# Kernel tuning notes

Measured on AMD Instinct MI355X. Metric: run time of the kernel, lower is better.

Reference implementation:

```python
import jax, jax.numpy as jnp
import numpy as np

B, L, C = 32, 64, 4


def setup_inputs() -> dict:
    key = jax.random.key(0)
    k_idx, k0, k1, k2, k3 = jax.random.split(key, 5)
    # One-hot encoded sequences, flattened to (B, L*C) as the layer expects.
    idx = jax.random.randint(k_idx, (B, L), 0, C)
    x_lc = jax.nn.one_hot(idx, C, dtype=jnp.float32).reshape(B, L * C)
    return {
        "x_lc": x_lc,
        "theta_0": jnp.zeros((1,), dtype=jnp.float32),  # Constant(0.0) init
        "theta_1": 0.05 * jax.random.normal(k1, (L, C), dtype=jnp.float32),
        "theta_2": 0.05 * jax.random.normal(k2, (L, C, L, C), dtype=jnp.float32),
        "theta_3": 0.05 * jax.random.normal(k3, (L, C, L, C, L, C), dtype=jnp.float32),
    }


def reference(x_lc, theta_0, theta_1, theta_2, theta_3):
    Lp, Cp = theta_1.shape
    xr = x_lc.reshape(-1, Lp, Cp)  # (B, L, C)
    pos = jnp.arange(Lp)
    # strict upper-triangular position masks: l0 < l1 (< l2)
    m2 = (pos[None, :] > pos[:, None]).astype(theta_2.dtype)      # (L, L)
    m3 = m2[:, :, None] * m2[None, :, :]                           # (L, L, L)
    # order 1: sum_{l,c} theta_1[l,c] x[b,l,c]
    phi = theta_0[0] + jnp.einsum('ua,bua->b', theta_1, xr)
    # order 2: sum over l0<l1 of theta_2 * x x
    phi = phi + jnp.einsum('uavc,uv,bua,bvc->b', theta_2, m2, xr, xr)
    # order 3: sum over l0<l1<l2 of theta_3 * x x x
    phi = phi + jnp.einsum('uavcwe,uvw,bua,bvc,bwe->b', theta_3, m3, xr, xr, xr)
    return phi.reshape(-1, 1)
```

## Files before the change

kernel.cpp:

```cpp
#include <hip/hip_runtime.h>

#define BB 32
#define LL 64
#define LC 256
#define NPAIR 2016
#define PPB 4
#define NBLK (NPAIR / PPB)


__global__ __launch_bounds__(256) void init_kernel(
    const float* __restrict__ x, const float* __restrict__ t0,
    const float* __restrict__ t1, float* __restrict__ out)
{
    const int tid = threadIdx.x;
    const int b = tid >> 3, k = tid & 7;
    const float4* __restrict__ x4 = (const float4*)x + b * 64;
    float s = 0.0f;
#pragma unroll
    for (int m = 0; m < 8; ++m) {
        const int l = 8 * m + k;
        float4 f = x4[l];
        int c = 0; float best = f.x;
        if (f.y > best) { best = f.y; c = 1; }
        if (f.z > best) { best = f.z; c = 2; }
        if (f.w > best) { best = f.w; c = 3; }
        s += t1[4 * l + c];
    }
    s += __shfl_down(s, 4, 8);
    s += __shfl_down(s, 2, 8);
    s += __shfl_down(s, 1, 8);
    if (k == 0) out[b] = s + t0[0];
}

__global__ __launch_bounds__(256) void pair_kernel(
    const float* __restrict__ x, const float* __restrict__ t2,
    const float* __restrict__ t3, float* __restrict__ out)
{
    const int tid = threadIdx.x;
    const int b = tid >> 3, k = tid & 7;
    const float4* __restrict__ x4 = (const float4*)x + b * 64;

    int c[8];
#pragma unroll
    for (int m = 0; m < 8; ++m) {
        float4 f = x4[8 * m + k];
        int ci = 0; float best = f.x;
        if (f.y > best) { best = f.y; ci = 1; }
        if (f.z > best) { best = f.z; ci = 2; }
        if (f.w > best) { best = f.w; ci = 3; }
        c[m] = ci;
    }

    const int tp0 = blockIdx.x * PPB;
    int v = (int)((1.0f + sqrtf(8.0f * (float)tp0 + 1.0f)) * 0.5f);
    while (v * (v - 1) / 2 > tp0) --v;
    while ((v + 1) * v / 2 <= tp0) ++v;
    int u = tp0 - v * (v - 1) / 2;

    float acc = 0.0f;
#pragma unroll
    for (int i = 0; i < PPB; ++i) {
        float4 fu = x4[u], fv = x4[v];
        int cu = 0; { float bst = fu.x;
            if (fu.y > bst) { bst = fu.y; cu = 1; }
            if (fu.z > bst) { bst = fu.z; cu = 2; }
            if (fu.w > bst) { bst = fu.w; cu = 3; } }
        int cv = 0; { float bst = fv.x;
            if (fv.y > bst) { bst = fv.y; cv = 1; }
            if (fv.z > bst) { bst = fv.z; cv = 2; }
            if (fv.w > bst) { bst = fv.w; cv = 3; } }
        const int pu = 4 * u + cu, pv = 4 * v + cv;

        const float4* __restrict__ row4 =
            (const float4*)(t3 + ((size_t)pu << 16) + ((size_t)pv << 8));
        if (k == 0) acc += t2[pu * LC + pv];

#pragma unroll
        for (int m = 0; m < 8; ++m) {
            const int w = 8 * m + k;
            float4 f = row4[w];
            const int ci = c[m];
            float lo = (ci & 1) ? f.y : f.x;
            float hi = (ci & 1) ? f.w : f.z;
            float val = (ci & 2) ? hi : lo;
            acc += (w > v) ? val : 0.0f;
        }

        ++u; if (u == v) { u = 0; ++v; }
    }

    acc += __shfl_down(acc, 4, 8);
    acc += __shfl_down(acc, 2, 8);
    acc += __shfl_down(acc, 1, 8);
    if (k == 0) atomicAdd(&out[b], acc);
}

extern "C" void kernel_launch(void* const* d_in, const int* in_sizes, int n_in,
                              void* d_out, int out_size, void* d_ws, size_t ws_size,
                              hipStream_t stream) {
    const float* x  = (const float*)d_in[0];
    const float* t0 = (const float*)d_in[1];
    const float* t1 = (const float*)d_in[2];
    const float* t2 = (const float*)d_in[3];
    const float* t3 = (const float*)d_in[4];
    float* out = (float*)d_out;
    (void)d_ws; (void)ws_size;

    init_kernel<<<1, 256, 0, stream>>>(x, t0, t1, out);
    pair_kernel<<<NBLK, 256, 0, stream>>>(x, t2, t3, out);
}
```

Baseline: 112.5 us.

## Fuse init and pair kernels into one cooperative kernel with grid-sync reduction

```diff
diff --git a/kernel.cpp b/kernel.cpp
--- a/kernel.cpp
+++ b/kernel.cpp
@@ -1,98 +1,105 @@
 #include <hip/hip_runtime.h>
+#include <hip/hip_cooperative_groups.h>
+
+namespace cg = cooperative_groups;
 
 #define BB 32
 #define LL 64
 #define LC 256
 #define NPAIR 2016
-#define PPB 4
+#define PPB 2
 #define NBLK (NPAIR / PPB)
+#define WSTR 1024
 
-
-__global__ __launch_bounds__(256) void init_kernel(
+__global__ __launch_bounds__(256, 4) void fused_kernel(
     const float* __restrict__ x, const float* __restrict__ t0,
-    const float* __restrict__ t1, float* __restrict__ out)
+    const float* __restrict__ t1, const float* __restrict__ t2,
+    const float* __restrict__ t3, float* __restrict__ ws,
+    float* __restrict__ out)
 {
     const int tid = threadIdx.x;
-    const int b = tid >> 3, k = tid & 7;
-    const float4* __restrict__ x4 = (const float4*)x + b * 64;
-    float s = 0.0f;
+    const int j = blockIdx.x;
+    __shared__ float wsum[4];
+
+    {
+        const int b = tid >> 3, k = tid & 7;
+        const float4* __restrict__ x4 = (const float4*)x + b * 64;
+
+        int c[8];
 #pragma unroll
-    for (int m = 0; m < 8; ++m) {
-        const int l = 8 * m + k;
-        float4 f = x4[l];
-        int c = 0; float best = f.x;
-        if (f.y > best) { best = f.y; c = 1; }
-        if (f.z > best) { best = f.z; c = 2; }
-        if (f.w > best) { best = f.w; c = 3; }
-        s += t1[4 * l + c];
-    }
-    s += __shfl_down(s, 4, 8);
-    s += __shfl_down(s, 2, 8);
-    s += __shfl_down(s, 1, 8);
-    if (k == 0) out[b] = s + t0[0];
-}
+        for (int m = 0; m < 8; ++m) {
+            float4 f = x4[8 * m + k];
+            int ci = 0; float best = f.x;
+            if (f.y > best) { best = f.y; ci = 1; }
+            if (f.z > best) { best = f.z; ci = 2; }
+            if (f.w > best) { best = f.w; ci = 3; }
+            c[m] = ci;
+        }
 
-__global__ __launch_bounds__(256) void pair_kernel(
-    const float* __restrict__ x, const float* __restrict__ t2,
-    const float* __restrict__ t3, float* __restrict__ out)
-{
-    const int tid = threadIdx.x;
-    const int b = tid >> 3, k = tid & 7;
-    const float4* __restrict__ x4 = (const float4*)x + b * 64;
+        const int tp0 = j * PPB;
+        int v = (int)((1.0f + sqrtf(8.0f * (float)tp0 + 1.0f)) * 0.5f);
+        while (v * (v - 1) / 2 > tp0) --v;
+        while ((v + 1) * v / 2 <= tp0) ++v;
+        int u = tp0 - v * (v - 1) / 2;
 
-    int c[8];
+        float acc = 0.0f;
 #pragma unroll
-    for (int m = 0; m < 8; ++m) {
-        float4 f = x4[8 * m + k];
-        int ci = 0; float best = f.x;
-        if (f.y > best) { best = f.y; ci = 1; }
-        if (f.z > best) { best = f.z; ci = 2; }
-        if (f.w > best) { best = f.w; ci = 3; }
-        c[m] = ci;
+        for (int i = 0; i < PPB; ++i) {
+            float4 fu = x4[u], fv = x4[v];
+            int cu = 0; { float bst = fu.x;
+                if (fu.y > bst) { bst = fu.y; cu = 1; }
+                if (fu.z > bst) { bst = fu.z; cu = 2; }
+                if (fu.w > bst) { bst = fu.w; cu = 3; } }
+            int cv = 0; { float bst = fv.x;
+                if (fv.y > bst) { bst = fv.y; cv = 1; }
+                if (fv.z > bst) { bst = fv.z; cv = 2; }
+                if (fv.w > bst) { bst = fv.w; cv = 3; } }
+            const int pu = 4 * u + cu, pv = 4 * v + cv;
+
+            const float4* __restrict__ row4 =
+                (const float4*)(t3 + ((size_t)pu << 16) + ((size_t)pv << 8));
+            if (k == 0) acc += t2[pu * LC + pv];
+
+#pragma unroll
+            for (int m = 0; m < 8; ++m) {
+                const int w = 8 * m + k;
+                float4 f = row4[w];
+                const int ci = c[m];
+                float lo = (ci & 1) ? f.y : f.x;
+                float hi = (ci & 1) ? f.w : f.z;
+                float val = (ci & 2) ? hi : lo;
+                acc += (w > v) ? val : 0.0f;
+            }
+
+            ++u; if (u == v) { u = 0; ++v; }
+        }
+
+        acc += __shfl_down(acc, 4, 8);
+        acc += __shfl_down(acc, 2, 8);
+        acc += __shfl_down(acc, 1, 8);
+        if (k == 0) ws[b * WSTR + j] = acc;
     }
 
-    const int tp0 = blockIdx.x * PPB;
-    int v = (int)((1.0f + sqrtf(8.0f * (float)tp0 + 1.0f)) * 0.5f);
-    while (v * (v - 1) / 2 > tp0) --v;
-    while ((v + 1) * v / 2 <= tp0) ++v;
-    int u = tp0 - v * (v - 1) / 2;
+    cg::this_grid().sync();
 
-    float acc = 0.0f;
-#pragma unroll
-    for (int i = 0; i < PPB; ++i) {
-        float4 fu = x4[u], fv = x4[v];
-        int cu = 0; { float bst = fu.x;
-            if (fu.y > bst) { bst = fu.y; cu = 1; }
-            if (fu.z > bst) { bst = fu.z; cu = 2; }
-            if (fu.w > bst) { bst = fu.w; cu = 3; } }
-        int cv = 0; { float bst = fv.x;
-            if (fv.y > bst) { bst = fv.y; cv = 1; }
-            if (fv.z > bst) { bst = fv.z; cv = 2; }
-            if (fv.w > bst) { bst = fv.w; cv = 3; } }
-        const int pu = 4 * u + cu, pv = 4 * v + cv;
-
-        const float4* __restrict__ row4 =
-            (const float4*)(t3 + ((size_t)pu << 16) + ((size_t)pv << 8));
-        if (k == 0) acc += t2[pu * LC + pv];
-
-#pragma unroll
-        for (int m = 0; m < 8; ++m) {
-            const int w = 8 * m + k;
-            float4 f = row4[w];
-            const int ci = c[m];
-            float lo = (ci & 1) ? f.y : f.x;
-            float hi = (ci & 1) ? f.w : f.z;
-            float val = (ci & 2) ? hi : lo;
-            acc += (w > v) ? val : 0.0f;
+    if (j < BB) {
+        const int b = j;
+        const float* __restrict__ wsb = ws + b * WSTR;
+        float s = 0.0f;
+        for (int p = tid; p < NBLK; p += 256) s += wsb[p];
+        if (tid < LL) {
+            float4 f = ((const float4*)x)[b * 64 + tid];
+            int c = 0; float best = f.x;
+            if (f.y > best) { best = f.y; c = 1; }
+            if (f.z > best) { best = f.z; c = 2; }
+            if (f.w > best) { best = f.w; c = 3; }
+            s += t1[4 * tid + c];
         }
-
-        ++u; if (u == v) { u = 0; ++v; }
+        for (int off = 32; off > 0; off >>= 1) s += __shfl_down(s, off, 64);
+        if ((tid & 63) == 0) wsum[tid >> 6] = s;
+        __syncthreads();
+        if (tid == 0) out[b] = wsum[0] + wsum[1] + wsum[2] + wsum[3] + t0[0];
     }
-
-    acc += __shfl_down(acc, 4, 8);
-    acc += __shfl_down(acc, 2, 8);
-    acc += __shfl_down(acc, 1, 8);
-    if (k == 0) atomicAdd(&out[b], acc);
 }
 
 extern "C" void kernel_launch(void* const* d_in, const int* in_sizes, int n_in,
@@ -104,8 +111,10 @@
     const float* t2 = (const float*)d_in[3];
     const float* t3 = (const float*)d_in[4];
     float* out = (float*)d_out;
-    (void)d_ws; (void)ws_size;
+    float* ws  = (float*)d_ws;
 
-    init_kernel<<<1, 256, 0, stream>>>(x, t0, t1, out);
-    pair_kernel<<<NBLK, 256, 0, stream>>>(x, t2, t3, out);
+    void* args[] = { (void*)&x, (void*)&t0, (void*)&t1, (void*)&t2,
+                     (void*)&t3, (void*)&ws, (void*)&out };
+    hipLaunchCooperativeKernel((const void*)fused_kernel,
+                               dim3(NBLK), dim3(256), args, 0, stream);
 }
```

After: 210.3 us. 1.87x slower.
